# Performance work log

Measured on AMD Instinct MI355X. Metric: run time of the kernel, lower is better.

Reference implementation:

```python
import jax, jax.numpy as jnp
import numpy as np

# SLAYER neuron params (from network.yaml defaults)
THETA = 10.0      # spike threshold
TAU_SR = 10.0     # synaptic (PSP) time constant
TAU_REF = 1.0     # refractory time constant
SCALE_REF = 2.0   # refractory strength (in units of theta)
TAU_RHO = 1.0     # surrogate-gradient width
SCALE_RHO = 1.0   # surrogate-gradient scale
TS = 1.0          # simulation timestep


@jax.custom_vjp
def spike_heaviside(u):
    # SLAYER spike generation: hard threshold in forward
    return (u >= THETA).astype(u.dtype)

def _spk_fwd(u):
    return spike_heaviside(u), u

def _spk_bwd(u, g):
    # SLAYER surrogate: rho(u) = (scaleRho/tauRho) * exp(-|u - theta| / tauRho)
    surr = (SCALE_RHO / TAU_RHO) * jnp.exp(-jnp.abs(u - THETA) / TAU_RHO)
    return (g * surr,)

spike_heaviside.defvjp(_spk_fwd, _spk_bwd)


def psp(x):
    """Temporal post-synaptic-potential filter (exponential synapse kernel).
    x: (B, T, F) -> (B, T, F);  p[t] = decay * p[t-1] + x[t]."""
    decay = jnp.exp(jnp.asarray(-TS / TAU_SR, x.dtype))
    def step(p, xt):
        p = decay * p + xt
        return p, p
    p0 = jnp.zeros((x.shape[0], x.shape[2]), x.dtype)
    _, ps = jax.lax.scan(step, p0, jnp.swapaxes(x, 0, 1))  # scan over T
    return jnp.swapaxes(ps, 0, 1)


def spike(u):
    """Thresholded spike generation with refractory feedback.
    u: (B, T, F) membrane input; refractory state subtracts 2*theta after a spike
    and decays with tauRef (SLAYER refractory response)."""
    decay_ref = jnp.exp(jnp.asarray(-TS / TAU_REF, u.dtype))
    def step(r, ut):
        v = ut + r
        s = spike_heaviside(v)
        r = decay_ref * (r - SCALE_REF * THETA * s)
        return r, s
    r0 = jnp.zeros((u.shape[0], u.shape[2]), u.dtype)
    _, ss = jax.lax.scan(step, r0, jnp.swapaxes(u, 0, 1))  # scan over T
    return jnp.swapaxes(ss, 0, 1)


def setup_inputs() -> dict:
    key = jax.random.key(0)
    k1, k2, k3 = jax.random.split(key, 3)
    B, T, F_IN, F_H, F_OUT = 64, 500, 1250, 512, 2
    x = (jax.random.uniform(k1, (B, T, F_IN)) < 0.1).astype(jnp.float32)
    W1 = jax.random.normal(k2, (F_H, F_IN), jnp.float32) * 0.05
    W2 = jax.random.normal(k3, (F_OUT, F_H), jnp.float32) * 0.05
    return {"x": x, "W1": W1, "W2": W2}


def reference(x, W1, W2):
    # layer 1: dense projection per timestep -> PSP filter -> spike
    s1 = spike(psp(jnp.einsum('btf,hf->bth', x, W1)))   # (B, T, 512)
    # layer 2
    out = spike(psp(jnp.einsum('bth,oh->bto', s1, W2))) # (B, T, 2)
    return out
```

## Files before the change

### kernel.cpp

```cpp
#include <hip/hip_runtime.h>
#include <hip/hip_bf16.h>
#include <cstdint>
#include <cstddef>

#define B_N   64
#define T_N   500
#define K_IN  1250
#define N_H   512
#define N_OUT 2
#define M_N   (B_N * T_N)

#define BM 128
#define BN 128
#define BK 32

static_assert(M_N % BM == 0, "M tiling");
static_assert(N_H % BN == 0, "N tiling");

typedef __attribute__((ext_vector_type(8))) short bf16x8;
typedef __attribute__((ext_vector_type(4))) float f32x4;

#define DECAY_SR  0.9048374180359595732f
#define DECAY_REF 0.3678794411714423216f
#define THETA 10.0f

__device__ __forceinline__ short f2bf(float f) {
  union { float f; uint32_t u; } v; v.f = f;
  uint32_t r = v.u + 0x7FFFu + ((v.u >> 16) & 1u);
  return (short)(r >> 16);
}
__device__ __forceinline__ float bf2f(short s) {
  union { uint32_t u; float f; } v;
  v.u = ((uint32_t)(uint16_t)s) << 16;
  return v.f;
}

__global__ __launch_bounds__(256) void gemm1_kernel(const float* __restrict__ X,
                                                    const float* __restrict__ W1,
                                                    float* __restrict__ U1) {
  __shared__ short As[BM][BK];
  __shared__ short Bs[BN][BK];
  const int tid  = threadIdx.x;
  const int bm   = blockIdx.x * BM;
  const int bn   = blockIdx.y * BN;
  const int w    = tid >> 6;
  const int lane = tid & 63;
  const int wr   = w >> 1;
  const int wc   = w & 1;
  const int lrow = lane & 15;
  const int lgrp = lane >> 4;

  f32x4 acc[4][4];
  #pragma unroll
  for (int i = 0; i < 4; ++i)
    #pragma unroll
    for (int j = 0; j < 4; ++j)
      acc[i][j] = (f32x4){0.f, 0.f, 0.f, 0.f};

  for (int k0 = 0; k0 < K_IN; k0 += BK) {
    #pragma unroll
    for (int rr = 0; rr < 4; ++rr) {
      int j   = rr * 256 + tid;
      int row = j >> 3;
      int kq  = (j & 7) * 4;
      int gk  = k0 + kq;
      const float* srcA = X  + (size_t)(bm + row) * K_IN + gk;
      const float* srcB = W1 + (size_t)(bn + row) * K_IN + gk;
      float a0, a1, a2, a3, b0, b1, b2, b3;
      if (gk + 3 < K_IN) {
        float2 x0 = *(const float2*)srcA;
        float2 x1 = *(const float2*)(srcA + 2);
        float2 y0 = *(const float2*)srcB;
        float2 y1 = *(const float2*)(srcB + 2);
        a0 = x0.x; a1 = x0.y; a2 = x1.x; a3 = x1.y;
        b0 = y0.x; b1 = y0.y; b2 = y1.x; b3 = y1.y;
      } else {
        a0 = (gk + 0 < K_IN) ? srcA[0] : 0.f;
        a1 = (gk + 1 < K_IN) ? srcA[1] : 0.f;
        a2 = (gk + 2 < K_IN) ? srcA[2] : 0.f;
        a3 = (gk + 3 < K_IN) ? srcA[3] : 0.f;
        b0 = (gk + 0 < K_IN) ? srcB[0] : 0.f;
        b1 = (gk + 1 < K_IN) ? srcB[1] : 0.f;
        b2 = (gk + 2 < K_IN) ? srcB[2] : 0.f;
        b3 = (gk + 3 < K_IN) ? srcB[3] : 0.f;
      }
      short4 ha; ha.x = f2bf(a0); ha.y = f2bf(a1); ha.z = f2bf(a2); ha.w = f2bf(a3);
      short4 hb; hb.x = f2bf(b0); hb.y = f2bf(b1); hb.z = f2bf(b2); hb.w = f2bf(b3);
      *(short4*)&As[row][kq] = ha;
      *(short4*)&Bs[row][kq] = hb;
    }
    __syncthreads();

    bf16x8 af[4], bfv[4];
    #pragma unroll
    for (int i = 0; i < 4; ++i) {
      af[i]  = *(const bf16x8*)&As[wr * 64 + i * 16 + lrow][lgrp * 8];
      bfv[i] = *(const bf16x8*)&Bs[wc * 64 + i * 16 + lrow][lgrp * 8];
    }
    #pragma unroll
    for (int i = 0; i < 4; ++i)
      #pragma unroll
      for (int j = 0; j < 4; ++j)
        acc[i][j] = __builtin_amdgcn_mfma_f32_16x16x32_bf16(af[i], bfv[j], acc[i][j], 0, 0, 0);
    __syncthreads();
  }

  #pragma unroll
  for (int i = 0; i < 4; ++i) {
    int rowb = bm + wr * 64 + i * 16 + lgrp * 4;
    #pragma unroll
    for (int j = 0; j < 4; ++j) {
      int col = bn + wc * 64 + j * 16 + lrow;
      #pragma unroll
      for (int r = 0; r < 4; ++r)
        U1[(size_t)(rowb + r) * N_H + col] = acc[i][j][r];
    }
  }
}

__global__ __launch_bounds__(256) void scan1_kernel(const float* __restrict__ U1,
                                                    short* __restrict__ S1) {
  int idx = blockIdx.x * 256 + threadIdx.x;
  int b = idx >> 9, h = idx & 511;
  const float* u = U1 + (size_t)b * T_N * N_H + h;
  short*       s = S1 + (size_t)b * T_N * N_H + h;
  float p = 0.f, r = 0.f;
  for (int t0 = 0; t0 < T_N; t0 += 10) {
    float buf[10];
    #pragma unroll
    for (int j = 0; j < 10; ++j) buf[j] = u[(size_t)(t0 + j) * N_H];
    #pragma unroll
    for (int j = 0; j < 10; ++j) {
      p = DECAY_SR * p + buf[j];
      float v = p + r;
      float sp = (v >= THETA) ? 1.f : 0.f;
      r = DECAY_REF * (r - 2.f * THETA * sp);
      s[(size_t)(t0 + j) * N_H] = (sp > 0.f) ? (short)0x3F80 : (short)0;
    }
  }
}

__global__ __launch_bounds__(256) void gemm2_kernel(const short* __restrict__ S1,
                                                    const float* __restrict__ W2,
                                                    float* __restrict__ U2) {
  int m    = blockIdx.x * 4 + (threadIdx.x >> 6);
  int lane = threadIdx.x & 63;
  const bf16x8 sv = *(const bf16x8*)&S1[(size_t)m * N_H + lane * 8];
  float a0 = 0.f, a1 = 0.f;
  #pragma unroll
  for (int j = 0; j < 8; ++j) {
    float sj = bf2f(sv[j]);
    a0 += sj * W2[lane * 8 + j];
    a1 += sj * W2[N_H + lane * 8 + j];
  }
  #pragma unroll
  for (int off = 32; off >= 1; off >>= 1) {
    a0 += __shfl_down(a0, off);
    a1 += __shfl_down(a1, off);
  }
  if (lane == 0) {
    U2[(size_t)m * 2]     = a0;
    U2[(size_t)m * 2 + 1] = a1;
  }
}

__global__ __launch_bounds__(128) void scan2_kernel(const float* __restrict__ U2,
                                                    float* __restrict__ OUT) {
  __shared__ float lu[T_N * 2];
  __shared__ float ls[T_N * 2];
  int b = blockIdx.x;
  const float* src = U2 + (size_t)b * T_N * 2;
  for (int i = threadIdx.x; i < T_N * 2; i += 128) lu[i] = src[i];
  __syncthreads();
  if (threadIdx.x < 2) {
    int o = threadIdx.x;
    float p = 0.f, r = 0.f;
    for (int t = 0; t < T_N; ++t) {
      p = DECAY_SR * p + lu[t * 2 + o];
      float v = p + r;
      float sp = (v >= THETA) ? 1.f : 0.f;
      r = DECAY_REF * (r - 2.f * THETA * sp);
      ls[t * 2 + o] = sp;
    }
  }
  __syncthreads();
  float* dst = OUT + (size_t)b * T_N * 2;
  for (int i = threadIdx.x; i < T_N * 2; i += 128) dst[i] = ls[i];
}

extern "C" void kernel_launch(void* const* d_in, const int* in_sizes, int n_in,
                              void* d_out, int out_size, void* d_ws, size_t ws_size,
                              hipStream_t stream) {
  const float* X  = (const float*)d_in[0];
  const float* W1 = (const float*)d_in[1];
  const float* W2 = (const float*)d_in[2];
  float* OUT = (float*)d_out;

  char* ws = (char*)d_ws;
  float* U1 = (float*)ws;
  short* S1 = (short*)(ws + (size_t)M_N * N_H * 4);
  float* U2 = (float*)(ws + (size_t)M_N * N_H * 6);

  gemm1_kernel<<<dim3(M_N / BM, N_H / BN), 256, 0, stream>>>(X, W1, U1);
  scan1_kernel<<<dim3((B_N * N_H) / 256), 256, 0, stream>>>(U1, S1);
  gemm2_kernel<<<dim3(M_N / 4), 256, 0, stream>>>(S1, W2, U2);
  scan2_kernel<<<dim3(B_N), 128, 0, stream>>>(U2, OUT);
}
```

Before: 404.8 us.

## Pre-convert W1 to bf16, double-buffer GEMM with direct LDS loads, bitpack spikes

A new kernel pre-converts W1 to padded bf16, which gemm1 then streams straight into swizzled, double-buffered shared memory with global_load_lds. X tiles are packed 8 values at a time into swizzled LDS. U1 is now stored as bf16 instead of fp32, and scan1 emits spike bitmasks via ballot, with software-pipelined loads, for gemm2 to read as bytes. Together these cut global traffic and hide load latency. Rounding the membrane input to bf16 before thresholding can flip spikes near theta.

Result: faster. 387.9 us (-4.2%).

```diff
diff --git a/kernel.cpp b/kernel.cpp
--- a/kernel.cpp
+++ b/kernel.cpp
@@ -6,16 +6,14 @@
 #define B_N   64
 #define T_N   500
 #define K_IN  1250
+#define KP    1280
 #define N_H   512
-#define N_OUT 2
-#define M_N   (B_N * T_N)
+#define M_N   32000
 
 #define BM 128
 #define BN 128
 #define BK 32
-
-static_assert(M_N % BM == 0, "M tiling");
-static_assert(N_H % BN == 0, "N tiling");
+#define NT (KP / BK)
 
 typedef __attribute__((ext_vector_type(8))) short bf16x8;
 typedef __attribute__((ext_vector_type(4))) float f32x4;
@@ -24,22 +22,32 @@
 #define DECAY_REF 0.3678794411714423216f
 #define THETA 10.0f
 
-__device__ __forceinline__ short f2bf(float f) {
-  union { float f; uint32_t u; } v; v.f = f;
-  uint32_t r = v.u + 0x7FFFu + ((v.u >> 16) & 1u);
-  return (short)(r >> 16);
-}
-__device__ __forceinline__ float bf2f(short s) {
-  union { uint32_t u; float f; } v;
-  v.u = ((uint32_t)(uint16_t)s) << 16;
-  return v.f;
+__device__ __forceinline__ unsigned short f2bf(float f) {
+  __hip_bfloat16 h = __float2bfloat16(f);
+  return *reinterpret_cast<unsigned short*>(&h);
+}
+__device__ __forceinline__ uint32_t f2bf2(float a, float b) {
+  float2 t; t.x = a; t.y = b;
+  __hip_bfloat162 h = __float22bfloat162_rn(t);
+  return *reinterpret_cast<uint32_t*>(&h);
+}
+__device__ __forceinline__ float bf2f(unsigned short s) {
+  union { uint32_t u; float f; } v; v.u = ((uint32_t)s) << 16; return v.f;
+}
+
+__global__ __launch_bounds__(256) void w1cvt_kernel(const float* __restrict__ W1,
+                                                    short* __restrict__ W1b) {
+  int k = blockIdx.x * 256 + threadIdx.x;
+  int n = blockIdx.y;
+  float v = (k < K_IN) ? W1[(size_t)n * K_IN + k] : 0.f;
+  W1b[(size_t)n * KP + k] = (short)f2bf(v);
 }
 
 __global__ __launch_bounds__(256) void gemm1_kernel(const float* __restrict__ X,
-                                                    const float* __restrict__ W1,
-                                                    float* __restrict__ U1) {
-  __shared__ short As[BM][BK];
-  __shared__ short Bs[BN][BK];
+                                                    const short* __restrict__ W1b,
+                                                    unsigned short* __restrict__ U1) {
+  __shared__ short As[2][BM * BK];
+  __shared__ short Bs[2][BN * BK];
   const int tid  = threadIdx.x;
   const int bm   = blockIdx.x * BM;
   const int bn   = blockIdx.y * BN;
@@ -57,101 +65,140 @@
     for (int j = 0; j < 4; ++j)
       acc[i][j] = (f32x4){0.f, 0.f, 0.f, 0.f};
 
-  for (int k0 = 0; k0 < K_IN; k0 += BK) {
-    #pragma unroll
-    for (int rr = 0; rr < 4; ++rr) {
-      int j   = rr * 256 + tid;
-      int row = j >> 3;
-      int kq  = (j & 7) * 4;
-      int gk  = k0 + kq;
-      const float* srcA = X  + (size_t)(bm + row) * K_IN + gk;
-      const float* srcB = W1 + (size_t)(bn + row) * K_IN + gk;
-      float a0, a1, a2, a3, b0, b1, b2, b3;
-      if (gk + 3 < K_IN) {
-        float2 x0 = *(const float2*)srcA;
-        float2 x1 = *(const float2*)(srcA + 2);
-        float2 y0 = *(const float2*)srcB;
-        float2 y1 = *(const float2*)(srcB + 2);
-        a0 = x0.x; a1 = x0.y; a2 = x1.x; a3 = x1.y;
-        b0 = y0.x; b1 = y0.y; b2 = y1.x; b3 = y1.y;
+  const int arow  = tid >> 2;
+  const int aslot = tid & 3;
+  const int bch0  = w * 2;
+  const int brow  = lane >> 2;
+  const int bslp  = lane & 3;
+
+  auto stage = [&](int buf, int k0) {
+    #pragma unroll
+    for (int c = 0; c < 2; ++c) {
+      int ch = bch0 + c;
+      int n  = ch * 16 + brow;
+      int ss = bslp ^ ((n >> 1) & 3);
+      const short* src = W1b + (size_t)(bn + n) * KP + k0 + ss * 8;
+      __builtin_amdgcn_global_load_lds(
+          (const __attribute__((address_space(1))) void*)src,
+          (__attribute__((address_space(3))) void*)&Bs[buf][ch * 512], 16, 0, 0);
+    }
+    #pragma unroll
+    for (int rr = 0; rr < 2; ++rr) {
+      int row = arow + rr * 64;
+      int gk  = k0 + aslot * 8;
+      const float* s = X + (size_t)(bm + row) * K_IN + gk;
+      float v0, v1, v2, v3, v4, v5, v6, v7;
+      if (gk + 7 < K_IN) {
+        float2 x0 = *(const float2*)(s);
+        float2 x1 = *(const float2*)(s + 2);
+        float2 x2 = *(const float2*)(s + 4);
+        float2 x3 = *(const float2*)(s + 6);
+        v0 = x0.x; v1 = x0.y; v2 = x1.x; v3 = x1.y;
+        v4 = x2.x; v5 = x2.y; v6 = x3.x; v7 = x3.y;
       } else {
-        a0 = (gk + 0 < K_IN) ? srcA[0] : 0.f;
-        a1 = (gk + 1 < K_IN) ? srcA[1] : 0.f;
-        a2 = (gk + 2 < K_IN) ? srcA[2] : 0.f;
-        a3 = (gk + 3 < K_IN) ? srcA[3] : 0.f;
-        b0 = (gk + 0 < K_IN) ? srcB[0] : 0.f;
-        b1 = (gk + 1 < K_IN) ? srcB[1] : 0.f;
-        b2 = (gk + 2 < K_IN) ? srcB[2] : 0.f;
-        b3 = (gk + 3 < K_IN) ? srcB[3] : 0.f;
+        v0 = (gk + 0 < K_IN) ? s[0] : 0.f;
+        v1 = (gk + 1 < K_IN) ? s[1] : 0.f;
+        v2 = (gk + 2 < K_IN) ? s[2] : 0.f;
+        v3 = (gk + 3 < K_IN) ? s[3] : 0.f;
+        v4 = (gk + 4 < K_IN) ? s[4] : 0.f;
+        v5 = (gk + 5 < K_IN) ? s[5] : 0.f;
+        v6 = (gk + 6 < K_IN) ? s[6] : 0.f;
+        v7 = (gk + 7 < K_IN) ? s[7] : 0.f;
       }
-      short4 ha; ha.x = f2bf(a0); ha.y = f2bf(a1); ha.z = f2bf(a2); ha.w = f2bf(a3);
-      short4 hb; hb.x = f2bf(b0); hb.y = f2bf(b1); hb.z = f2bf(b2); hb.w = f2bf(b3);
-      *(short4*)&As[row][kq] = ha;
-      *(short4*)&Bs[row][kq] = hb;
-    }
-    __syncthreads();
-
-    bf16x8 af[4], bfv[4];
+      uint4 pk;
+      pk.x = f2bf2(v0, v1); pk.y = f2bf2(v2, v3);
+      pk.z = f2bf2(v4, v5); pk.w = f2bf2(v6, v7);
+      *(uint4*)&As[buf][row * BK + ((aslot ^ ((row >> 1) & 3)) * 8)] = pk;
+    }
+  };
+
+  stage(0, 0);
+  __syncthreads();
+  int pb = 0;
+  for (int t = 0; t < NT; ++t) {
+    if (t + 1 < NT) stage(pb ^ 1, (t + 1) * BK);
+    bf16x8 af[4], bv[4];
     #pragma unroll
     for (int i = 0; i < 4; ++i) {
-      af[i]  = *(const bf16x8*)&As[wr * 64 + i * 16 + lrow][lgrp * 8];
-      bfv[i] = *(const bf16x8*)&Bs[wc * 64 + i * 16 + lrow][lgrp * 8];
+      int r = wr * 64 + i * 16 + lrow;
+      af[i] = *(const bf16x8*)&As[pb][r * BK + ((lgrp ^ ((r >> 1) & 3)) * 8)];
+    }
+    #pragma unroll
+    for (int j = 0; j < 4; ++j) {
+      int r = wc * 64 + j * 16 + lrow;
+      bv[j] = *(const bf16x8*)&Bs[pb][r * BK + ((lgrp ^ ((r >> 1) & 3)) * 8)];
     }
     #pragma unroll
     for (int i = 0; i < 4; ++i)
       #pragma unroll
       for (int j = 0; j < 4; ++j)
-        acc[i][j] = __builtin_amdgcn_mfma_f32_16x16x32_bf16(af[i], bfv[j], acc[i][j], 0, 0, 0);
+        acc[i][j] = __builtin_amdgcn_mfma_f32_16x16x32_bf16(af[i], bv[j], acc[i][j], 0, 0, 0);
     __syncthreads();
+    pb ^= 1;
   }
 
   #pragma unroll
   for (int i = 0; i < 4; ++i) {
-    int rowb = bm + wr * 64 + i * 16 + lgrp * 4;
+    int row0 = bm + wr * 64 + i * 16 + lgrp * 4;
     #pragma unroll
     for (int j = 0; j < 4; ++j) {
       int col = bn + wc * 64 + j * 16 + lrow;
       #pragma unroll
       for (int r = 0; r < 4; ++r)
-        U1[(size_t)(rowb + r) * N_H + col] = acc[i][j][r];
-    }
-  }
-}
-
-__global__ __launch_bounds__(256) void scan1_kernel(const float* __restrict__ U1,
-                                                    short* __restrict__ S1) {
-  int idx = blockIdx.x * 256 + threadIdx.x;
-  int b = idx >> 9, h = idx & 511;
-  const float* u = U1 + (size_t)b * T_N * N_H + h;
-  short*       s = S1 + (size_t)b * T_N * N_H + h;
+        U1[(size_t)(row0 + r) * N_H + col] = f2bf(acc[i][j][r]);
+    }
+  }
+}
+
+__global__ __launch_bounds__(128) void scan1_kernel(const unsigned short* __restrict__ U1,
+                                                    unsigned long long* __restrict__ S1m) {
+  int idx  = blockIdx.x * 128 + threadIdx.x;
+  int b    = idx >> 9, h = idx & 511;
+  int lane = threadIdx.x & 63;
+  const unsigned short* u = U1 + (size_t)b * T_N * N_H + h;
+  unsigned long long* mout = S1m + (size_t)b * T_N * 8 + (h >> 6);
   float p = 0.f, r = 0.f;
-  for (int t0 = 0; t0 < T_N; t0 += 10) {
-    float buf[10];
-    #pragma unroll
-    for (int j = 0; j < 10; ++j) buf[j] = u[(size_t)(t0 + j) * N_H];
+  float bufA[10], bufB[10];
+
+  auto load = [&](float* buf, int t0) {
+    #pragma unroll
+    for (int j = 0; j < 10; ++j) buf[j] = bf2f(u[(size_t)(t0 + j) * N_H]);
+  };
+  auto proc = [&](const float* buf, int t0) {
     #pragma unroll
     for (int j = 0; j < 10; ++j) {
       p = DECAY_SR * p + buf[j];
       float v = p + r;
-      float sp = (v >= THETA) ? 1.f : 0.f;
-      r = DECAY_REF * (r - 2.f * THETA * sp);
-      s[(size_t)(t0 + j) * N_H] = (sp > 0.f) ? (short)0x3F80 : (short)0;
-    }
-  }
-}
-
-__global__ __launch_bounds__(256) void gemm2_kernel(const short* __restrict__ S1,
+      bool sp = (v >= THETA);
+      r = DECAY_REF * (r - (sp ? 2.f * THETA : 0.f));
+      unsigned long long bal = __ballot(sp);
+      if (lane == 0) mout[(size_t)(t0 + j) * 8] = bal;
+    }
+  };
+
+  load(bufA, 0);
+  for (int g = 0; g < 25; ++g) {
+    int ta = g * 20, tb = ta + 10;
+    load(bufB, tb);
+    proc(bufA, ta);
+    if (g < 24) load(bufA, tb + 10);
+    proc(bufB, tb);
+  }
+}
+
+__global__ __launch_bounds__(256) void gemm2_kernel(const unsigned char* __restrict__ S1b,
                                                     const float* __restrict__ W2,
                                                     float* __restrict__ U2) {
   int m    = blockIdx.x * 4 + (threadIdx.x >> 6);
   int lane = threadIdx.x & 63;
-  const bf16x8 sv = *(const bf16x8*)&S1[(size_t)m * N_H + lane * 8];
+  unsigned int byte = S1b[(size_t)m * 64 + lane];
   float a0 = 0.f, a1 = 0.f;
   #pragma unroll
   for (int j = 0; j < 8; ++j) {
-    float sj = bf2f(sv[j]);
-    a0 += sj * W2[lane * 8 + j];
-    a1 += sj * W2[N_H + lane * 8 + j];
+    int h = lane * 8 + j;
+    float sel = ((byte >> j) & 1u) ? 1.f : 0.f;
+    a0 += sel * W2[h];
+    a1 += sel * W2[N_H + h];
   }
   #pragma unroll
   for (int off = 32; off >= 1; off >>= 1) {
@@ -197,12 +244,14 @@
   float* OUT = (float*)d_out;
 
   char* ws = (char*)d_ws;
-  float* U1 = (float*)ws;
-  short* S1 = (short*)(ws + (size_t)M_N * N_H * 4);
-  float* U2 = (float*)(ws + (size_t)M_N * N_H * 6);
-
-  gemm1_kernel<<<dim3(M_N / BM, N_H / BN), 256, 0, stream>>>(X, W1, U1);
-  scan1_kernel<<<dim3((B_N * N_H) / 256), 256, 0, stream>>>(U1, S1);
-  gemm2_kernel<<<dim3(M_N / 4), 256, 0, stream>>>(S1, W2, U2);
+  short*              W1b = (short*)ws;
+  unsigned short*     U1  = (unsigned short*)(ws + 1310720);
+  unsigned long long* S1m = (unsigned long long*)(ws + 34078720);
+  float*              U2  = (float*)(ws + 36126720);
+
+  w1cvt_kernel<<<dim3(KP / 256, N_H), 256, 0, stream>>>(W1, W1b);
+  gemm1_kernel<<<dim3(M_N / BM, N_H / BN), 256, 0, stream>>>(X, W1b, U1);
+  scan1_kernel<<<dim3((B_N * N_H) / 128), 128, 0, stream>>>(U1, S1m);
+  gemm2_kernel<<<dim3(M_N / 4), 256, 0, stream>>>((const unsigned char*)S1m, W2, U2);
   scan2_kernel<<<dim3(B_N), 128, 0, stream>>>(U2, OUT);
 }
```
